# Kernel tuning notes

Hardware: AMD Instinct MI355X
Metric: run time of the kernel (lower is better)

## Reference

```python
import jax, jax.numpy as jnp
import numpy as np

B, S, D = 4, 2048, 1024

def setup_inputs() -> dict:
    key = jax.random.key(0)
    kx, kk, kq, kv = jax.random.split(key, 4)
    scale = 1.0 / np.sqrt(D)
    x = jax.random.normal(kx, (B, S, D), dtype=jnp.float32)
    # nn.Linear weights, applied as x @ W.T; init with small scale like torch default
    Wk = jax.random.normal(kk, (D, D), dtype=jnp.float32) * scale
    Wq = jax.random.normal(kq, (D, D), dtype=jnp.float32) * scale
    Wv = jax.random.normal(kv, (D, D), dtype=jnp.float32) * scale
    return {"x": x, "Wk": Wk, "Wq": Wq, "Wv": Wv}

def reference(x, Wk, Wq, Wv):
    # k/q/v: (B, S, D) @ (D, D_out) -- Linear applies W as x @ W.T
    k = jnp.einsum('bsd,kd->bsk', x, Wk)
    q = jnp.einsum('bsd,kd->bsk', x, Wq)
    v = jnp.einsum('bsd,vd->bsv', x, Wv)
    # scaled dot-product scores: (B, S, S)
    scores = jnp.einsum('bqk,bsk->bqs', q, k) / jnp.sqrt(jnp.asarray(k.shape[-1], x.dtype))
    # causal mask: allow j <= i (upper-right masked out)
    S_len = x.shape[1]
    causal = jnp.tril(jnp.ones((S_len, S_len), dtype=bool))
    scores = jnp.where(causal[None, :, :], scores, jnp.asarray(-jnp.inf, x.dtype))
    weights = jax.nn.softmax(scores, axis=-1)
    # dropout is identity in eval / p used as deterministic baseline
    out = jnp.einsum('bqs,bsv->bqv', weights, v)
    return out
```

## Files before the change

kernel.cpp:

```cpp
#include <hip/hip_runtime.h>

typedef __attribute__((ext_vector_type(8))) short bf16x8;
typedef __attribute__((ext_vector_type(4))) float f32x4;
typedef __attribute__((ext_vector_type(4))) unsigned short u16x4;
typedef __attribute__((ext_vector_type(8))) unsigned short u16x8;

#define MFMA16(a, b, c) __builtin_amdgcn_mfma_f32_16x16x32_bf16((a), (b), (c), 0, 0, 0)

__device__ __forceinline__ ushort f2bf(float f) {
    unsigned u = __float_as_uint(f);
    unsigned r = (u + 0x7FFFu + ((u >> 16) & 1u)) >> 16;
    return (ushort)r;
}
__device__ __forceinline__ float bf2f(ushort s) {
    return __uint_as_float(((unsigned)s) << 16);
}

__device__ __forceinline__ void async16(const ushort* g, ushort* l) {
    __builtin_amdgcn_global_load_lds(
        (const __attribute__((address_space(1))) unsigned*)g,
        (__attribute__((address_space(3))) unsigned*)l, 16, 0, 0);
}

#define SBAR()  __builtin_amdgcn_s_barrier()
#define SCHED() __builtin_amdgcn_sched_barrier(0)

__global__ __launch_bounds__(256) void cvt_bf16(
    const float* __restrict__ x, const float* __restrict__ wv,
    ushort* __restrict__ xb, ushort* __restrict__ wvb)
{
    const size_t XN = (size_t)8192 * 1024;
    size_t idx = ((size_t)blockIdx.x * 256 + threadIdx.x) * 8;
    const float* s;
    ushort* d;
    if (idx < XN) { s = x + idx; d = xb + idx; }
    else          { s = wv + (idx - XN); d = wvb + (idx - XN); }
    float4 a = *(const float4*)s;
    float4 b = *(const float4*)(s + 4);
    u16x8 p;
    p[0] = f2bf(a.x); p[1] = f2bf(a.y); p[2] = f2bf(a.z); p[3] = f2bf(a.w);
    p[4] = f2bf(b.x); p[5] = f2bf(b.y); p[6] = f2bf(b.z); p[7] = f2bf(b.w);
    *(u16x8*)d = p;
}

__global__ __launch_bounds__(256) void cvt_transpose(
    const float* __restrict__ w0, const float* __restrict__ w1,
    ushort* __restrict__ t0, ushort* __restrict__ t1)
{
    const float* src = blockIdx.z ? w1 : w0;
    ushort*      dst = blockIdx.z ? t1 : t0;
    __shared__ float t[32][33];
    const int e0 = blockIdx.x * 32, d0 = blockIdx.y * 32;
    const int tx = threadIdx.x, ty = threadIdx.y;
#pragma unroll
    for (int r = 0; r < 4; ++r)
        t[ty + 8 * r][tx] = src[(size_t)(e0 + ty + 8 * r) * 1024 + d0 + tx];
    __syncthreads();
#pragma unroll
    for (int r = 0; r < 4; ++r)
        dst[(size_t)(d0 + ty + 8 * r) * 1024 + e0 + tx] = f2bf(t[tx][ty + 8 * r]);
}

__device__ __forceinline__ void mma_tile(
    const ushort* __restrict__ A, int lda, int abase,
    const ushort* __restrict__ B, int ldb, int bbase,
    int ktiles,
    ushort* As, ushort* Bs, f32x4 (&acc)[4][4])
{
    const int tid  = threadIdx.x;
    const int lane = tid & 63, wid = tid >> 6;
    const int wr = wid >> 1, wc = wid & 1;
    const int lrow = lane & 15, kgrp = lane >> 4;
    const int ci = lane >> 3;
    const int cc = (lane & 7) * 8;

#pragma unroll
    for (int m = 0; m < 4; ++m)
#pragma unroll
        for (int n = 0; n < 4; ++n) acc[m][n] = (f32x4){0.f, 0.f, 0.f, 0.f};

    for (int kt = 0; kt < ktiles; ++kt) {
        const int k0 = kt * 64;
#pragma unroll
        for (int i = 0; i < 4; ++i) {
            const int r = (wid * 4 + i) * 8 + ci;
            async16(&A[(size_t)(abase + r) * lda + k0 + cc], &As[(wid * 4 + i) * 512]);
            async16(&B[(size_t)(bbase + r) * ldb + k0 + cc], &Bs[(wid * 4 + i) * 512]);
        }
        __syncthreads();
#pragma unroll
        for (int kk = 0; kk < 2; ++kk) {
            bf16x8 af[4], bfr[4];
#pragma unroll
            for (int m = 0; m < 4; ++m)
                af[m] = *(const bf16x8*)&As[(wr * 64 + m * 16 + lrow) * 64 + kk * 32 + kgrp * 8];
#pragma unroll
            for (int n = 0; n < 4; ++n)
                bfr[n] = *(const bf16x8*)&Bs[(wc * 64 + n * 16 + lrow) * 64 + kk * 32 + kgrp * 8];
#pragma unroll
            for (int m = 0; m < 4; ++m)
#pragma unroll
                for (int n = 0; n < 4; ++n)
                    acc[m][n] = MFMA16(af[m], bfr[n], acc[m][n]);
        }
        __syncthreads();
    }
}

__device__ __forceinline__ void mma256(
    const ushort* __restrict__ A, int lda, int abase,
    const ushort* __restrict__ B, int ldb, int bbase,
    int NT, ushort* As, ushort* Bs, f32x4 (&acc)[8][4])
{
    const int tid  = threadIdx.x;
    const int lane = tid & 63, w = tid >> 6;
    const int wr = w >> 2, wc = w & 3;
    const int lrow = lane & 15, kgrp = lane >> 4;
    const int srr = lane >> 2;
    const int scc = (lane & 3) * 8;

    auto stage = [&](int t, int isB, int kk) {
        const ushort* src = isB ? B : A;
        const int ld = isB ? ldb : lda;
        const int rb = isB ? bbase : abase;
        ushort* slot = (isB ? Bs : As) + (size_t)(((t & 1) * 2 + kk)) * 8192;
#pragma unroll
        for (int i = 0; i < 2; ++i) {
            const int r = (w * 2 + i) * 16 + srr;
            async16(&src[(size_t)(rb + r) * ld + t * 64 + kk * 32 + scc],
                    slot + (w * 2 + i) * 512);
        }
    };

#pragma unroll
    for (int m = 0; m < 8; ++m)
#pragma unroll
        for (int n = 0; n < 4; ++n) acc[m][n] = (f32x4){0.f, 0.f, 0.f, 0.f};

    stage(0, 0, 0); stage(0, 1, 0); stage(0, 0, 1); stage(0, 1, 1);
    if (NT > 1) {
        stage(1, 0, 0); stage(1, 1, 0);
        asm volatile("s_waitcnt vmcnt(4)" ::: "memory");
    } else {
        asm volatile("s_waitcnt vmcnt(0)" ::: "memory");
    }
    SCHED();
    SBAR();
    SCHED();

    for (int t = 0; t < NT; ++t) {
        ushort* Ab = As + (size_t)(t & 1) * 2 * 8192;
        ushort* Bb = Bs + (size_t)(t & 1) * 2 * 8192;
        bf16x8 af[8], bfr[2];

#pragma unroll
        for (int m = 0; m < 8; ++m)
            af[m] = *(const bf16x8*)&Ab[(wr * 128 + m * 16 + lrow) * 32 + kgrp * 8];
#pragma unroll
        for (int n = 0; n < 2; ++n)
            bfr[n] = *(const bf16x8*)&Bb[(wc * 64 + n * 16 + lrow) * 32 + kgrp * 8];
        if (t + 1 < NT) stage(t + 1, 0, 1);
        SBAR(); SCHED();
        __builtin_amdgcn_s_setprio(1);
#pragma unroll
        for (int m = 0; m < 8; ++m) {
            acc[m][0] = MFMA16(af[m], bfr[0], acc[m][0]);
            acc[m][1] = MFMA16(af[m], bfr[1], acc[m][1]);
        }
        __builtin_amdgcn_s_setprio(0);
        SBAR(); SCHED();

#pragma unroll
        for (int n = 0; n < 2; ++n)
            bfr[n] = *(const bf16x8*)&Bb[(wc * 64 + (2 + n) * 16 + lrow) * 32 + kgrp * 8];
        if (t + 1 < NT) stage(t + 1, 1, 1);
        SBAR(); SCHED();
        __builtin_amdgcn_s_setprio(1);
#pragma unroll
        for (int m = 0; m < 8; ++m) {
            acc[m][2] = MFMA16(af[m], bfr[0], acc[m][2]);
            acc[m][3] = MFMA16(af[m], bfr[1], acc[m][3]);
        }
        __builtin_amdgcn_s_setprio(0);
        SBAR(); SCHED();

#pragma unroll
        for (int m = 0; m < 8; ++m)
            af[m] = *(const bf16x8*)&Ab[8192 + (wr * 128 + m * 16 + lrow) * 32 + kgrp * 8];
#pragma unroll
        for (int n = 0; n < 2; ++n)
            bfr[n] = *(const bf16x8*)&Bb[8192 + (wc * 64 + n * 16 + lrow) * 32 + kgrp * 8];
        if (t + 2 < NT) stage(t + 2, 0, 0);
        SBAR(); SCHED();
        __builtin_amdgcn_s_setprio(1);
#pragma unroll
        for (int m = 0; m < 8; ++m) {
            acc[m][0] = MFMA16(af[m], bfr[0], acc[m][0]);
            acc[m][1] = MFMA16(af[m], bfr[1], acc[m][1]);
        }
        __builtin_amdgcn_s_setprio(0);
        SBAR(); SCHED();

#pragma unroll
        for (int n = 0; n < 2; ++n)
            bfr[n] = *(const bf16x8*)&Bb[8192 + (wc * 64 + (2 + n) * 16 + lrow) * 32 + kgrp * 8];
        if (t + 2 < NT) {
            stage(t + 2, 1, 0);
            asm volatile("s_waitcnt vmcnt(4)" ::: "memory");
        } else if (t + 1 < NT) {
            asm volatile("s_waitcnt vmcnt(0)" ::: "memory");
        }
        SCHED();
        SBAR(); SCHED();
        __builtin_amdgcn_s_setprio(1);
#pragma unroll
        for (int m = 0; m < 8; ++m) {
            acc[m][2] = MFMA16(af[m], bfr[0], acc[m][2]);
            acc[m][3] = MFMA16(af[m], bfr[1], acc[m][3]);
        }
        __builtin_amdgcn_s_setprio(0);
        SBAR(); SCHED();
    }
}

__global__ __launch_bounds__(256) void m_gemm(
    const ushort* __restrict__ Wkt, const ushort* __restrict__ Wqt,
    ushort* __restrict__ Mtr)
{
    __shared__ ushort As[128 * 64];
    __shared__ ushort Bs[128 * 64];
    const int fbase = blockIdx.x * 128;
    const int dbase = blockIdx.y * 128;

    f32x4 acc[4][4];
    mma_tile(Wkt, 1024, fbase, Wqt, 1024, dbase, 16, As, Bs, acc);

    const int lane = threadIdx.x & 63, wid = threadIdx.x >> 6;
    const int wr = wid >> 1, wc = wid & 1;
    const int lrow = lane & 15, kgrp = lane >> 4;
#pragma unroll
    for (int m = 0; m < 4; ++m)
#pragma unroll
        for (int n = 0; n < 4; ++n)
#pragma unroll
            for (int r = 0; r < 4; ++r) {
                const int gf = fbase + wr * 64 + m * 16 + kgrp * 4 + r;
                const int gd = dbase + wc * 64 + n * 16 + lrow;
                Mtr[(size_t)gf * 1024 + gd] = f2bf(acc[m][n][r] * 0.03125f);
            }
}

__global__ __launch_bounds__(512, 2) void tv_gemm8(
    const ushort* __restrict__ xb, const ushort* __restrict__ Mtr,
    const ushort* __restrict__ Wvb,
    ushort* __restrict__ Tb, ushort* __restrict__ Vt)
{
    __shared__ ushort As[2 * 2 * 8192];
    __shared__ ushort Bs[2 * 2 * 8192];

    const int z = blockIdx.z;
    const ushort* Bmat = z ? Wvb : Mtr;
    const int mbase = blockIdx.x * 256;
    const int nbase = blockIdx.y * 256;

    f32x4 acc[8][4];
    mma256(xb, 1024, mbase, Bmat, 1024, nbase, 16, As, Bs, acc);

    const int lane = threadIdx.x & 63, w = threadIdx.x >> 6;
    const int wr = w >> 2, wc = w & 3;
    const int lrow = lane & 15, kgrp = lane >> 4;

    if (z == 1) {
        const int b  = mbase >> 11;
        const int s0 = mbase & 2047;
        ushort* VtB = Vt + (size_t)b * 1024 * 2048;
#pragma unroll
        for (int m = 0; m < 8; ++m)
#pragma unroll
            for (int n = 0; n < 4; ++n) {
                u16x4 pk;
#pragma unroll
                for (int r = 0; r < 4; ++r) pk[r] = f2bf(acc[m][n][r]);
                const int d = nbase + wc * 64 + n * 16 + lrow;
                const int s = s0 + wr * 128 + m * 16 + kgrp * 4;
                *(u16x4*)&VtB[(size_t)d * 2048 + s] = pk;
            }
    } else {
#pragma unroll
        for (int m = 0; m < 8; ++m)
#pragma unroll
            for (int n = 0; n < 4; ++n)
#pragma unroll
                for (int r = 0; r < 4; ++r) {
                    const int gr = mbase + wr * 128 + m * 16 + kgrp * 4 + r;
                    const int gc = nbase + wc * 64 + n * 16 + lrow;
                    Tb[(size_t)gr * 1024 + gc] = f2bf(acc[m][n][r]);
                }
    }
}

__global__ __launch_bounds__(512, 2) void scores_gemm8(
    const ushort* __restrict__ Tb, const ushort* __restrict__ xb,
    ushort* __restrict__ Sall)
{
    __shared__ ushort As[2 * 2 * 8192];
    __shared__ ushort Bs[2 * 2 * 8192];

    ushort* S = Sall + (size_t)blockIdx.y * 2048 * 2048;
    const int rb = blockIdx.y * 2048;

    int t = blockIdx.x;
    int it = (int)((sqrtf(8.0f * (float)t + 1.0f) - 1.0f) * 0.5f);
    while ((it + 1) * (it + 2) / 2 <= t) ++it;
    while (it * (it + 1) / 2 > t) --it;
    const int jt = t - it * (it + 1) / 2;
    const int ibase = it * 256, jbase = jt * 256;

    f32x4 acc[8][4];
    mma256(Tb, 1024, rb + ibase, xb, 1024, rb + jbase, 16, As, Bs, acc);

    const int lane = threadIdx.x & 63, w = threadIdx.x >> 6;
    const int wr = w >> 2, wc = w & 3;
    const int lrow = lane & 15, kgrp = lane >> 4;
#pragma unroll
    for (int m = 0; m < 8; ++m)
#pragma unroll
        for (int n = 0; n < 4; ++n)
#pragma unroll
            for (int r = 0; r < 4; ++r) {
                const int gi = ibase + wr * 128 + m * 16 + kgrp * 4 + r;
                const int gj = jbase + wc * 64 + n * 16 + lrow;
                S[(size_t)gi * 2048 + gj] = f2bf(acc[m][n][r]);
            }
}

__global__ __launch_bounds__(256) void softmax_rows(ushort* __restrict__ Sall)
{
    ushort* S = Sall + (size_t)blockIdx.y * 2048 * 2048;
    const int i   = blockIdx.x;
    const int tid = threadIdx.x;
    const int j0  = tid * 8;

    union { uint4 v; ushort u[8]; } pk;
    const bool anyvalid = (j0 <= i);
    if (anyvalid) pk.v = *(const uint4*)&S[(size_t)i * 2048 + j0];

    float f[8];
    float mx = -INFINITY;
#pragma unroll
    for (int e = 0; e < 8; ++e) {
        float v = (anyvalid && (j0 + e <= i)) ? bf2f(pk.u[e]) : -INFINITY;
        f[e] = v;
        mx = fmaxf(mx, v);
    }
#pragma unroll
    for (int off = 1; off < 64; off <<= 1) mx = fmaxf(mx, __shfl_xor(mx, off));
    __shared__ float redm[4];
    if ((tid & 63) == 0) redm[tid >> 6] = mx;
    __syncthreads();
    mx = fmaxf(fmaxf(redm[0], redm[1]), fmaxf(redm[2], redm[3]));

    float s = 0.f;
#pragma unroll
    for (int e = 0; e < 8; ++e) {
        float p = __expf(f[e] - mx);
        f[e] = p;
        s += p;
    }
#pragma unroll
    for (int off = 1; off < 64; off <<= 1) s += __shfl_xor(s, off);
    __shared__ float reds[4];
    if ((tid & 63) == 0) reds[tid >> 6] = s;
    __syncthreads();
    s = reds[0] + reds[1] + reds[2] + reds[3];

    const float inv = 1.0f / s;
#pragma unroll
    for (int e = 0; e < 8; ++e) pk.u[e] = f2bf(f[e] * inv);
    *(uint4*)&S[(size_t)i * 2048 + j0] = pk.v;
}

__global__ __launch_bounds__(256) void pv_gemm(
    const ushort* __restrict__ Pall, const ushort* __restrict__ Vtall,
    float* __restrict__ Oall)
{
    __shared__ ushort As[128 * 64];
    __shared__ ushort Bs[128 * 64];

    const ushort* P  = Pall  + (size_t)blockIdx.z * 2048 * 2048;
    const ushort* Vt = Vtall + (size_t)blockIdx.z * 1024 * 2048;
    float*        O  = Oall  + (size_t)blockIdx.z * 2048 * 1024;

    const int it = 15 - blockIdx.x;
    const int ibase = it * 128;
    const int nbase = blockIdx.y * 128;
    const int ktiles = 2 * (it + 1);

    f32x4 acc[4][4];
    mma_tile(P, 2048, ibase, Vt, 2048, nbase, ktiles, As, Bs, acc);

    const int lane = threadIdx.x & 63, wid = threadIdx.x >> 6;
    const int wr = wid >> 1, wc = wid & 1;
    const int lrow = lane & 15, kgrp = lane >> 4;
#pragma unroll
    for (int m = 0; m < 4; ++m)
#pragma unroll
        for (int n = 0; n < 4; ++n)
#pragma unroll
            for (int r = 0; r < 4; ++r) {
                const int gi = ibase + wr * 64 + m * 16 + kgrp * 4 + r;
                const int gc = nbase + wc * 64 + n * 16 + lrow;
                O[(size_t)gi * 1024 + gc] = acc[m][n][r];
            }
}

extern "C" void kernel_launch(void* const* d_in, const int* in_sizes, int n_in,
                              void* d_out, int out_size, void* d_ws, size_t ws_size,
                              hipStream_t stream)
{
    (void)in_sizes; (void)n_in; (void)out_size; (void)ws_size;
    const float* x  = (const float*)d_in[0];
    const float* Wk = (const float*)d_in[1];
    const float* Wq = (const float*)d_in[2];
    const float* Wv = (const float*)d_in[3];
    float* out = (float*)d_out;

    const size_t M1 = (size_t)1024 * 1024;
    ushort* ws  = (ushort*)d_ws;
    ushort* xb  = ws;
    ushort* Tb  = xb  + 8 * M1;
    ushort* Vt  = Tb  + 8 * M1;
    ushort* Sb  = Vt  + 8 * M1;
    ushort* Wkt = Sb  + 16 * M1;
    ushort* Wqt = Wkt + M1;
    ushort* Wvb = Wqt + M1;
    ushort* Mtr = Wvb + M1;

    cvt_transpose<<<dim3(32, 32, 2), dim3(32, 8), 0, stream>>>(Wk, Wq, Wkt, Wqt);
    cvt_bf16<<<4608, 256, 0, stream>>>(x, Wv, xb, Wvb);
    m_gemm<<<dim3(8, 8), 256, 0, stream>>>(Wkt, Wqt, Mtr);
    tv_gemm8<<<dim3(32, 4, 2), 512, 0, stream>>>(xb, Mtr, Wvb, Tb, Vt);
    scores_gemm8<<<dim3(36, 4), 512, 0, stream>>>(Tb, xb, Sb);
    softmax_rows<<<dim3(2048, 4), 256, 0, stream>>>(Sb);
    pv_gemm<<<dim3(16, 8, 4), 256, 0, stream>>>(Sb, Vt, out);
}
```

Measured before the change: 177.0 us.

## Replace PV GEMM with 8-wave 256x128 tiled kernel using double-buffered async staging

Replaces the 128x128 four-wave PV GEMM with a 512-thread kernel that computes 256x128 output tiles. It uses a new pipelined mainloop that stages half-K slices asynchronously into double-buffered LDS and interleaves MFMA phases with barriers. The larger tile raises operand reuse per LDS load and halves the number of blocks. In exchange the grid shrinks to 256 blocks with causal imbalance at a coarser granularity, which may hurt load balance across CUs.

```diff
diff --git a/kernel.cpp b/kernel.cpp
--- a/kernel.cpp
+++ b/kernel.cpp
@@ -223,6 +223,105 @@
     }
 }
 
+__device__ __forceinline__ void mma256x128(
+    const ushort* __restrict__ A, int lda, int abase,
+    const ushort* __restrict__ B, int ldb, int bbase,
+    int NT, ushort* As, ushort* Bs, f32x4 (&acc)[8][2])
+{
+    const int tid  = threadIdx.x;
+    const int lane = tid & 63, w = tid >> 6;
+    const int wr = w >> 2, wc = w & 3;
+    const int lrow = lane & 15, kgrp = lane >> 4;
+    const int srr = lane >> 2;
+    const int scc = (lane & 3) * 8;
+
+    auto stageA = [&](int t, int kk) {
+        ushort* slot = As + (size_t)((t & 1) * 2 + kk) * 8192;
+#pragma unroll
+        for (int i = 0; i < 2; ++i) {
+            const int r = (w * 2 + i) * 16 + srr;
+            async16(&A[(size_t)(abase + r) * lda + t * 64 + kk * 32 + scc],
+                    slot + (w * 2 + i) * 512);
+        }
+    };
+    auto stageB = [&](int t, int kk) {
+        ushort* slot = Bs + (size_t)((t & 1) * 2 + kk) * 4096;
+        const int r = w * 16 + srr;
+        async16(&B[(size_t)(bbase + r) * ldb + t * 64 + kk * 32 + scc],
+                slot + w * 512);
+    };
+
+#pragma unroll
+    for (int m = 0; m < 8; ++m)
+#pragma unroll
+        for (int n = 0; n < 2; ++n) acc[m][n] = (f32x4){0.f, 0.f, 0.f, 0.f};
+
+    stageA(0, 0); stageB(0, 0); stageA(0, 1); stageB(0, 1);
+    if (NT > 1) {
+        stageA(1, 0); stageB(1, 0);
+        asm volatile("s_waitcnt vmcnt(3)" ::: "memory");
+    } else {
+        asm volatile("s_waitcnt vmcnt(0)" ::: "memory");
+    }
+    SCHED();
+    SBAR();
+    SCHED();
+
+    for (int t = 0; t < NT; ++t) {
+        ushort* Ab = As + (size_t)(t & 1) * 16384;
+        ushort* Bb = Bs + (size_t)(t & 1) * 8192;
+        bf16x8 af[8], bfr;
+
+#pragma unroll
+        for (int m = 0; m < 8; ++m)
+            af[m] = *(const bf16x8*)&Ab[(wr * 128 + m * 16 + lrow) * 32 + kgrp * 8];
+        bfr = *(const bf16x8*)&Bb[(wc * 32 + lrow) * 32 + kgrp * 8];
+        if (t + 1 < NT) stageA(t + 1, 1);
+        SBAR(); SCHED();
+        __builtin_amdgcn_s_setprio(1);
+#pragma unroll
+        for (int m = 0; m < 8; ++m) acc[m][0] = MFMA16(af[m], bfr, acc[m][0]);
+        __builtin_amdgcn_s_setprio(0);
+        SBAR(); SCHED();
+
+        bfr = *(const bf16x8*)&Bb[(wc * 32 + 16 + lrow) * 32 + kgrp * 8];
+        if (t + 1 < NT) stageB(t + 1, 1);
+        SBAR(); SCHED();
+        __builtin_amdgcn_s_setprio(1);
+#pragma unroll
+        for (int m = 0; m < 8; ++m) acc[m][1] = MFMA16(af[m], bfr, acc[m][1]);
+        __builtin_amdgcn_s_setprio(0);
+        SBAR(); SCHED();
+
+#pragma unroll
+        for (int m = 0; m < 8; ++m)
+            af[m] = *(const bf16x8*)&Ab[8192 + (wr * 128 + m * 16 + lrow) * 32 + kgrp * 8];
+        bfr = *(const bf16x8*)&Bb[4096 + (wc * 32 + lrow) * 32 + kgrp * 8];
+        if (t + 2 < NT) stageA(t + 2, 0);
+        SBAR(); SCHED();
+        __builtin_amdgcn_s_setprio(1);
+#pragma unroll
+        for (int m = 0; m < 8; ++m) acc[m][0] = MFMA16(af[m], bfr, acc[m][0]);
+        __builtin_amdgcn_s_setprio(0);
+        SBAR(); SCHED();
+
+        bfr = *(const bf16x8*)&Bb[4096 + (wc * 32 + 16 + lrow) * 32 + kgrp * 8];
+        if (t + 2 < NT) {
+            stageB(t + 2, 0);
+            asm volatile("s_waitcnt vmcnt(3)" ::: "memory");
+        } else if (t + 1 < NT) {
+            asm volatile("s_waitcnt vmcnt(0)" ::: "memory");
+        }
+        SCHED();
+        SBAR(); SCHED();
+        __builtin_amdgcn_s_setprio(1);
+#pragma unroll
+        for (int m = 0; m < 8; ++m) acc[m][1] = MFMA16(af[m], bfr, acc[m][1]);
+        __builtin_amdgcn_s_setprio(0);
+        SBAR(); SCHED();
+    }
+}
+
 __global__ __launch_bounds__(256) void m_gemm(
     const ushort* __restrict__ Wkt, const ushort* __restrict__ Wqt,
     ushort* __restrict__ Mtr)
@@ -380,36 +479,36 @@
     *(uint4*)&S[(size_t)i * 2048 + j0] = pk.v;
 }
 
-__global__ __launch_bounds__(256) void pv_gemm(
+__global__ __launch_bounds__(512, 2) void pv_gemm8(
     const ushort* __restrict__ Pall, const ushort* __restrict__ Vtall,
     float* __restrict__ Oall)
 {
-    __shared__ ushort As[128 * 64];
-    __shared__ ushort Bs[128 * 64];
+    __shared__ ushort As[2 * 2 * 8192];
+    __shared__ ushort Bs[2 * 2 * 4096];
 
     const ushort* P  = Pall  + (size_t)blockIdx.z * 2048 * 2048;
     const ushort* Vt = Vtall + (size_t)blockIdx.z * 1024 * 2048;
     float*        O  = Oall  + (size_t)blockIdx.z * 2048 * 1024;
 
-    const int it = 15 - blockIdx.x;
-    const int ibase = it * 128;
+    const int it = 7 - blockIdx.x;
+    const int ibase = it * 256;
     const int nbase = blockIdx.y * 128;
-    const int ktiles = 2 * (it + 1);
-
-    f32x4 acc[4][4];
-    mma_tile(P, 2048, ibase, Vt, 2048, nbase, ktiles, As, Bs, acc);
-
-    const int lane = threadIdx.x & 63, wid = threadIdx.x >> 6;
-    const int wr = wid >> 1, wc = wid & 1;
-    const int lrow = lane & 15, kgrp = lane >> 4;
-#pragma unroll
-    for (int m = 0; m < 4; ++m)
-#pragma unroll
-        for (int n = 0; n < 4; ++n)
+    const int NT = 4 * (it + 1);
+
+    f32x4 acc[8][2];
+    mma256x128(P, 2048, ibase, Vt, 2048, nbase, NT, As, Bs, acc);
+
+    const int lane = threadIdx.x & 63, w = threadIdx.x >> 6;
+    const int wr = w >> 2, wc = w & 3;
+    const int lrow = lane & 15, kgrp = lane >> 4;
+#pragma unroll
+    for (int m = 0; m < 8; ++m)
+#pragma unroll
+        for (int n = 0; n < 2; ++n)
 #pragma unroll
             for (int r = 0; r < 4; ++r) {
-                const int gi = ibase + wr * 64 + m * 16 + kgrp * 4 + r;
-                const int gc = nbase + wc * 64 + n * 16 + lrow;
+                const int gi = ibase + wr * 128 + m * 16 + kgrp * 4 + r;
+                const int gc = nbase + wc * 32 + n * 16 + lrow;
                 O[(size_t)gi * 1024 + gc] = acc[m][n][r];
             }
 }
@@ -442,5 +541,5 @@
     tv_gemm8<<<dim3(32, 4, 2), 512, 0, stream>>>(xb, Mtr, Wvb, Tb, Vt);
     scores_gemm8<<<dim3(36, 4), 512, 0, stream>>>(Tb, xb, Sb);
     softmax_rows<<<dim3(2048, 4), 256, 0, stream>>>(Sb);
-    pv_gemm<<<dim3(16, 8, 4), 256, 0, stream>>>(Sb, Vt, out);
-}
+    pv_gemm8<<<dim3(8, 8, 4), 512, 0, stream>>>(Sb, Vt, out);
+}
```

After: 181.0 us. 1.02x slower.
